# Kernel tuning notes

Measured on AMD Instinct MI355X. Metric: run time of the kernel, lower is better.

The kernel has to match this reference:

```python
import jax, jax.numpy as jnp
import numpy as np

D_MODEL = 1024
NUM_HEADS = 16
HEAD_DIM = D_MODEL // NUM_HEADS
ROPE_BASE = 10000.0


def _rotate_half(x):
    x1, x2 = jnp.split(x, 2, axis=-1)
    return jnp.concatenate([-x2, x1], axis=-1)


def _rope_cache(seq_len, head_dim, dtype):
    half = head_dim // 2
    inv_freq = 1.0 / (ROPE_BASE ** (jnp.arange(half, dtype=jnp.float32) / float(half)))
    t = jnp.arange(seq_len, dtype=jnp.float32)
    freqs = t[:, None] * inv_freq[None, :]          # [s, half]
    emb = jnp.concatenate([freqs, freqs], axis=-1)   # [s, head_dim]
    cos = jnp.cos(emb)[None, None, :, :].astype(dtype)  # [1,1,s,d]
    sin = jnp.sin(emb)[None, None, :, :].astype(dtype)
    return cos, sin


def setup_inputs() -> dict:
    key = jax.random.key(0)
    k1, k2, k3 = jax.random.split(key, 3)
    b, s = 4, 2048
    x = jax.random.normal(k1, (b, s, D_MODEL), dtype=jnp.float32)
    mask = jnp.ones((b, s), dtype=jnp.float32)
    Wqkv = jax.random.normal(k2, (D_MODEL, 3 * D_MODEL), dtype=jnp.float32) * (D_MODEL ** -0.5)
    Wout = jax.random.normal(k3, (D_MODEL, D_MODEL), dtype=jnp.float32) * (D_MODEL ** -0.5)
    return {"x": x, "mask": mask, "Wqkv": Wqkv, "Wout": Wout}


def reference(x, mask, Wqkv, Wout):
    b, s, _ = x.shape
    qkv = x @ Wqkv                                   # [b,s,3*d_model]
    q, k, v = jnp.split(qkv, 3, axis=-1)

    def split_heads(t):
        return t.reshape(b, s, NUM_HEADS, HEAD_DIM).transpose(0, 2, 1, 3)  # [b,h,s,d]

    q, k, v = map(split_heads, (q, k, v))
    cos, sin = _rope_cache(s, HEAD_DIM, x.dtype)
    q = q * cos + _rotate_half(q) * sin
    k = k * cos + _rotate_half(k) * sin

    scale = HEAD_DIM ** -0.5
    logits = jnp.einsum('bhid,bhjd->bhij', q, k) * scale
    logits = logits + (1.0 - mask)[:, None, None, :] * -1e9
    attn = jax.nn.softmax(logits, axis=-1)
    out = jnp.einsum('bhij,bhjd->bhid', attn, v)     # [b,h,s,d]
    out = out.transpose(0, 2, 1, 3).reshape(b, s, D_MODEL)
    return out @ Wout
```

## Files before the change

### kernel.cpp

```cpp
#include <hip/hip_runtime.h>

typedef unsigned short u16;
typedef unsigned int u32;
typedef int i32x2 __attribute__((ext_vector_type(2)));
typedef float f32x4 __attribute__((ext_vector_type(4)));
typedef float f32x16 __attribute__((ext_vector_type(16)));
typedef __bf16 bf16x8 __attribute__((ext_vector_type(8)));
typedef unsigned short u16x8 __attribute__((ext_vector_type(8)));
typedef unsigned short u16x4 __attribute__((ext_vector_type(4)));
typedef unsigned int u32x4 __attribute__((ext_vector_type(4)));

#define S_ 2048
#define DM 1024

#define LDS_U32(p) ((__attribute__((address_space(3))) unsigned int*)(p))
#define GLB_U32(p) ((const __attribute__((address_space(1))) unsigned int*)(p))

__device__ __forceinline__ u16 f2bf(float f) {
    unsigned int u = __float_as_uint(f);
    u += 0x7fffu + ((u >> 16) & 1u);
    return (u16)(u >> 16);
}
__device__ __forceinline__ float bf2f(u16 s) {
    return __uint_as_float(((unsigned int)s) << 16);
}
__device__ __forceinline__ float fast_exp2(float x) {
#if __has_builtin(__builtin_amdgcn_exp2f)
    return __builtin_amdgcn_exp2f(x);
#else
    return __expf(x * 0.69314718056f);
#endif
}

__global__ __launch_bounds__(256) void f32_to_bf16_kernel(const float* __restrict__ in,
                                                          u16* __restrict__ o, int n) {
    int i = (blockIdx.x * 256 + threadIdx.x) << 2;
    if (i >= n) return;
    float4 f = *(const float4*)&in[i];
    u16x4 r;
    r[0] = f2bf(f.x); r[1] = f2bf(f.y); r[2] = f2bf(f.z); r[3] = f2bf(f.w);
    *(u16x4*)&o[i] = r;
}

__global__ __launch_bounds__(256) void transpose_w(const float* __restrict__ W,
                                                   u16* __restrict__ Wt, int K, int N) {
    __shared__ float tile[32][33];
    int nb = blockIdx.x << 5, kb = blockIdx.y << 5;
    int tx = threadIdx.x & 31, ty = threadIdx.x >> 5;
#pragma unroll
    for (int r = 0; r < 32; r += 8)
        tile[ty + r][tx] = W[(size_t)(kb + ty + r) * N + nb + tx];
    __syncthreads();
#pragma unroll
    for (int r = 0; r < 32; r += 8)
        Wt[(size_t)(nb + ty + r) * K + kb + tx] = f2bf(tile[tx][ty + r]);
}


#define ABLK(B, KK) ((B) * 32768 + (KK) * 8192)
#define BBLK(B, KK) ((B) * 32768 + 16384 + (KK) * 8192)

template <int MODE>
__global__ __launch_bounds__(512, 2) void gemm256(const u16* __restrict__ A,
                                                  const u16* __restrict__ Bt,
                                                  float* __restrict__ Cf,
                                                  u16* __restrict__ Qp, u16* __restrict__ Kp,
                                                  u16* __restrict__ Vtp,
                                                  int M, int N, int K) {
    __shared__ __align__(16) u16 lds[65536];
    const int tid = threadIdx.x, wave = tid >> 6, lane = tid & 63;
    const int Ntiles = N >> 8;
    const int cpx = gridDim.x >> 3;
    const int bid = (int)blockIdx.x;
    const int wg = (bid & 7) * cpx + (bid >> 3);
    const int mt = wg / Ntiles, nt = wg % Ntiles;
    const int m0 = mt << 8, n0 = nt << 8;
    const int wm = (wave >> 2) << 7, wn = (wave & 3) << 6;
    const int lr = lane & 15, lu = lane >> 4;

    const int NT = K >> 6;
    const int NIT = K >> 7;

    f32x4 acc[8][4] = {};

    const int srow0 = wave * 16 + (lane >> 2);
    const int scole = (((lane & 3) ^ ((lane >> 3) & 3)) << 3);

#define STAGE(BLK, MAT, ROW0, KCOL)                                                           \
    {                                                                                         \
        _Pragma("unroll") for (int l = 0; l < 2; ++l) {                                       \
            const u16* src = &(MAT)[(size_t)((ROW0) + srow0 + l * 128) * K + (KCOL) + scole];  \
            __builtin_amdgcn_global_load_lds(GLB_U32(src),                                    \
                LDS_U32(&lds[(BLK) + l * 4096 + wave * 512]), 16, 0, 0);                      \
        }                                                                                     \
    }

#define LDFRAG(BLK, ROW) \
    __builtin_bit_cast(bf16x8, *(const u16x8*)&lds[(BLK) + (ROW) * 32 + ((lu ^ (((ROW) >> 1) & 3)) << 3)])

#define PHASE(BUF, IH, KK, LOADB, SBLK, SMAT, SROW0, SKT, SKK, DOVM_END)                  \
    {                                                                                     \
        _Pragma("unroll") for (int ii = 0; ii < 4; ++ii) {                                \
            int row = wm + ((IH) * 4 + ii) * 16 + lr;                                     \
            af[ii] = LDFRAG(ABLK(BUF, KK), row);                                          \
        }                                                                                 \
        if (LOADB) {                                                                      \
            _Pragma("unroll") for (int j = 0; j < 4; ++j) {                               \
                int row = wn + j * 16 + lr;                                               \
                bfv[j] = LDFRAG(BBLK(BUF, KK), row);                                      \
            }                                                                             \
        }                                                                                 \
        STAGE(SBLK, SMAT, SROW0, (((SKT) & (NT - 1)) << 6) + ((SKK) << 5));               \
        asm volatile("s_barrier" ::: "memory");                                           \
        asm volatile("s_waitcnt lgkmcnt(0)" ::: "memory");                                \
        __builtin_amdgcn_sched_barrier(0);                                                \
        __builtin_amdgcn_s_setprio(1);                                                    \
        _Pragma("unroll") for (int ii = 0; ii < 4; ++ii)                                  \
            _Pragma("unroll") for (int j = 0; j < 4; ++j)                                 \
                acc[(IH) * 4 + ii][j] = __builtin_amdgcn_mfma_f32_16x16x32_bf16(          \
                    af[ii], bfv[j], acc[(IH) * 4 + ii][j], 0, 0, 0);                      \
        __builtin_amdgcn_s_setprio(0);                                                    \
        if (DOVM_END) asm volatile("s_waitcnt vmcnt(8)" ::: "memory");                    \
        asm volatile("s_barrier" ::: "memory");                                           \
    }

    STAGE(ABLK(0, 0), A, m0, 0);
    STAGE(BBLK(0, 0), Bt, n0, 0);
    STAGE(ABLK(0, 1), A, m0, 32);
    STAGE(BBLK(0, 1), Bt, n0, 32);
    STAGE(ABLK(1, 0), A, m0, 64);
    STAGE(BBLK(1, 0), Bt, n0, 64);
    asm volatile("s_waitcnt vmcnt(8)" ::: "memory");
    asm volatile("s_barrier" ::: "memory");

    for (int t = 0; t < NIT; ++t) {
        const int kt = 2 * t;
        bf16x8 af[4], bfv[4];
        PHASE(0, 0, 0, true,  ABLK(1, 1), A,  m0, kt + 1, 1, false);
        PHASE(0, 1, 0, false, BBLK(1, 1), Bt, n0, kt + 1, 1, true);
        PHASE(0, 0, 1, true,  ABLK(0, 0), A,  m0, kt + 2, 0, false);
        PHASE(0, 1, 1, false, BBLK(0, 0), Bt, n0, kt + 2, 0, true);
        PHASE(1, 0, 0, true,  ABLK(0, 1), A,  m0, kt + 2, 1, false);
        PHASE(1, 1, 0, false, BBLK(0, 1), Bt, n0, kt + 2, 1, true);
        PHASE(1, 0, 1, true,  ABLK(1, 0), A,  m0, kt + 3, 0, false);
        PHASE(1, 1, 1, false, BBLK(1, 0), Bt, n0, kt + 3, 0, true);
    }

    if (MODE == 0) {
        const int t = (n0 + wn) >> 10;
        if (t < 2) {
            const float LN1E4_32 = 9.210340371976184f / 32.0f;
            const float invf0 = __expf(-(float)lr * LN1E4_32);
            const float invf1 = __expf(-(float)(lr + 16) * LN1E4_32);
#pragma unroll
            for (int i = 0; i < 8; ++i) {
                const int rbase = m0 + wm + (i << 4) + ((lane >> 4) << 2);
#pragma unroll
                for (int jj = 0; jj < 4; ++jj) {
                    const float s = (float)((rbase + jj) & (S_ - 1));
                    float sn0, c0, sn1, c1;
                    __sincosf(s * invf0, &sn0, &c0);
                    __sincosf(s * invf1, &sn1, &c1);
                    const float v0 = acc[i][0][jj], v1 = acc[i][1][jj];
                    const float v2 = acc[i][2][jj], v3 = acc[i][3][jj];
                    acc[i][0][jj] = v0 * c0 - v2 * sn0;
                    acc[i][2][jj] = v2 * c0 + v0 * sn0;
                    acc[i][1][jj] = v1 * c1 - v3 * sn1;
                    acc[i][3][jj] = v3 * c1 + v1 * sn1;
                }
            }
            u16* P = (t == 0) ? Qp : Kp;
#pragma unroll
            for (int i = 0; i < 8; ++i) {
#pragma unroll
                for (int j = 0; j < 4; ++j) {
                    int rbase = m0 + wm + (i << 4) + ((lane >> 4) << 2);
                    int col = n0 + wn + (j << 4) + lr;
                    int h = (col & 1023) >> 6, d = col & 63;
#pragma unroll
                    for (int jj = 0; jj < 4; ++jj) {
                        int row = rbase + jj;
                        int b = row >> 11, s = row & 2047;
                        P[((size_t)((b << 4) + h) * S_ + s) * 64 + d] = f2bf(acc[i][j][jj]);
                    }
                }
            }
        } else {
#pragma unroll
            for (int i = 0; i < 8; ++i) {
                const int rbase = m0 + wm + (i << 4) + ((lane >> 4) << 2);
                const int b = rbase >> 11, sb = rbase & 2047;
#pragma unroll
                for (int j = 0; j < 4; ++j) {
                    int col = n0 + wn + (j << 4) + lr;
                    int h = (col & 1023) >> 6, d = col & 63;
                    u16x4 pk;
#pragma unroll
                    for (int jj = 0; jj < 4; ++jj) pk[jj] = f2bf(acc[i][j][jj]);
                    *(u16x4*)&Vtp[((size_t)((b << 4) + h) * 64 + d) * S_ + sb] = pk;
                }
            }
        }
    } else {
#pragma unroll
        for (int i = 0; i < 8; ++i)
#pragma unroll
            for (int j = 0; j < 4; ++j) {
                int rbase = m0 + wm + (i << 4) + ((lane >> 4) << 2);
                int col = n0 + wn + (j << 4) + lr;
#pragma unroll
                for (int jj = 0; jj < 4; ++jj)
                    Cf[(size_t)(rbase + jj) * N + col] = acc[i][j][jj];
            }
    }
#undef PHASE
#undef LDFRAG
#undef STAGE
}

__device__ __forceinline__ void softmax_chain(f32x16* p, f32x16* acc, f32x16& accS,
                                              float& m_run, u32* wa, u32* wb,
                                              const float* madd_tile, bool hasmask,
                                              float* bcast_w, int c, int hi) {
    if (hasmask) {
#pragma unroll
        for (int tt = 0; tt < 2; ++tt)
#pragma unroll
            for (int rq = 0; rq < 4; ++rq) {
                float4 mf = *(const float4*)&madd_tile[tt * 32 + rq * 8 + hi * 4];
                p[tt][4 * rq + 0] += mf.x;
                p[tt][4 * rq + 1] += mf.y;
                p[tt][4 * rq + 2] += mf.z;
                p[tt][4 * rq + 3] += mf.w;
            }
    }

    float tm[16];
#pragma unroll
    for (int r = 0; r < 16; ++r) tm[r] = fmaxf(p[0][r], p[1][r]);
    float a0 = fmaxf(fmaxf(tm[0], tm[1]), tm[2]);
    float a1 = fmaxf(fmaxf(tm[3], tm[4]), tm[5]);
    float a2 = fmaxf(fmaxf(tm[6], tm[7]), tm[8]);
    float a3 = fmaxf(fmaxf(tm[9], tm[10]), tm[11]);
    float a4 = fmaxf(fmaxf(tm[12], tm[13]), tm[14]);
    float b0 = fmaxf(fmaxf(a0, a1), a2);
    float b1 = fmaxf(fmaxf(a3, a4), tm[15]);
    float mx = fmaxf(b0, b1);
    {
        i32x2 mm = __builtin_amdgcn_permlane32_swap(__float_as_int(mx), __float_as_int(mx), false, false);
        mx = fmaxf(__int_as_float(mm[0]), __int_as_float(mm[1]));
    }

    if (!__all(mx - m_run <= 8.0f)) {
        float mnew = fmaxf(m_run, mx);
        float alpha = fast_exp2(m_run - mnew);
        m_run = mnew;
        bcast_w[c] = alpha;
        float avf[16];
#pragma unroll
        for (int rq = 0; rq < 4; ++rq) {
            float4 t4 = *(const float4*)&bcast_w[rq * 8 + hi * 4];
            avf[4 * rq + 0] = t4.x; avf[4 * rq + 1] = t4.y;
            avf[4 * rq + 2] = t4.z; avf[4 * rq + 3] = t4.w;
        }
#pragma unroll
        for (int r = 0; r < 16; ++r) {
            acc[0][r] *= avf[r];
            acc[1][r] *= avf[r];
            accS[r]   *= avf[r];
        }
    }

#pragma unroll
    for (int tt = 0; tt < 2; ++tt)
#pragma unroll
        for (int r = 0; r < 16; ++r)
            p[tt][r] = fast_exp2(p[tt][r] - m_run);

#pragma unroll
    for (int tt = 0; tt < 2; ++tt)
#pragma unroll
        for (int rq = 0; rq < 4; ++rq) {
            float e0 = p[tt][4 * rq + 0], e1 = p[tt][4 * rq + 1];
            float e2 = p[tt][4 * rq + 2], e3 = p[tt][4 * rq + 3];
            u32 w0, w1;
            asm("v_cvt_pk_bf16_f32 %0, %1, %2" : "=v"(w0) : "v"(e0), "v"(e1));
            asm("v_cvt_pk_bf16_f32 %0, %1, %2" : "=v"(w1) : "v"(e2), "v"(e3));
            wa[4 * tt + rq] = w0;
            wb[4 * tt + rq] = w1;
        }
}

__global__ __launch_bounds__(256, 2) void attn_kernel(const u16* __restrict__ q,
                                                      const u16* __restrict__ k,
                                                      const u16* __restrict__ vt,
                                                      const float* __restrict__ mask,
                                                      u16* __restrict__ outp) {
    __shared__ __align__(16) u16 Kl[2][64 * 64];
    __shared__ __align__(16) u16 Vl[2][64 * 64];
    __shared__ float madd2[2][64];
    __shared__ float bcast[4][32];

    const int tid = threadIdx.x, wave = tid >> 6, lane = tid & 63;
    const int c = lane & 31, hi = lane >> 5, c7 = c & 7;
    const int bh = blockIdx.x & 63, qt = blockIdx.x >> 6;
    const int b = bh >> 4, h = bh & 15;
    const size_t base = (size_t)bh * (S_ * 64);
    const int qrowA = (qt << 8) + (wave << 5) + c;
    const int qrowB = qrowA + 128;

    const float QS = 0.18033688f;

    bf16x8 qfA[4], qfB[4];
#pragma unroll
    for (int j = 0; j < 4; ++j) {
        u16x8 rawA = *(const u16x8*)&q[base + (size_t)qrowA * 64 + j * 16 + hi * 8];
        u16x8 rawB = *(const u16x8*)&q[base + (size_t)qrowB * 64 + j * 16 + hi * 8];
        u16x8 scA, scB;
#pragma unroll
        for (int e = 0; e < 8; ++e) {
            scA[e] = f2bf(bf2f(rawA[e]) * QS);
            scB[e] = f2bf(bf2f(rawB[e]) * QS);
        }
        qfA[j] = __builtin_bit_cast(bf16x8, scA);
        qfB[j] = __builtin_bit_cast(bf16x8, scB);
    }

    u16x8 ou;
#pragma unroll
    for (int e = 0; e < 8; ++e) ou[e] = 0x3F80;
    const bf16x8 onesf = __builtin_bit_cast(bf16x8, ou);

    f32x16 accA[2] = {}, accB[2] = {};
    f32x16 accSA = {}, accSB = {};
    float m_runA = -1e30f, m_runB = -1e30f;

    const int sr = tid >> 2, su = (tid & 3) << 1;
    const int so0 = sr * 64 + ((su ^ (sr & 7)) << 3);
    const int so1 = sr * 64 + (((su + 1) ^ (sr & 7)) << 3);

    u16x8 kc0 = *(const u16x8*)&k[base + (size_t)sr * 64 + su * 8];
    u16x8 kc1 = *(const u16x8*)&k[base + (size_t)sr * 64 + su * 8 + 8];
    u16x8 vc0 = *(const u16x8*)&vt[base + (size_t)sr * S_ + su * 8];
    u16x8 vc1 = *(const u16x8*)&vt[base + (size_t)sr * S_ + su * 8 + 8];
    float mval = (tid < 64) ? mask[b * S_ + tid] : 1.0f;

    for (int t = 0; t < 32; ++t) {
        const int bi = t & 1;
        u16* Kb = &Kl[bi][0];
        u16* Vb = &Vl[bi][0];
        *(u16x8*)&Kb[so0] = kc0;
        *(u16x8*)&Kb[so1] = kc1;
        *(u16x8*)&Vb[so0] = vc0;
        *(u16x8*)&Vb[so1] = vc1;
        if (tid < 64) madd2[bi][tid] = (1.0f - mval) * -1.44269504e9f;
        if (t + 1 < 32) {
            const int kn = (t + 1) << 6;
            kc0 = *(const u16x8*)&k[base + (size_t)(kn + sr) * 64 + su * 8];
            kc1 = *(const u16x8*)&k[base + (size_t)(kn + sr) * 64 + su * 8 + 8];
            vc0 = *(const u16x8*)&vt[base + (size_t)sr * S_ + kn + su * 8];
            vc1 = *(const u16x8*)&vt[base + (size_t)sr * S_ + kn + su * 8 + 8];
            mval = (tid < 64) ? mask[b * S_ + kn + tid] : 1.0f;
        }
        __syncthreads();

        f32x16 pA[2] = {}, pB[2] = {};
        __builtin_amdgcn_s_setprio(1);
#pragma unroll
        for (int j = 0; j < 4; ++j) {
            const int uo = ((2 * j + hi) ^ c7) << 3;
            bf16x8 ka  = __builtin_bit_cast(bf16x8, *(const u16x8*)&Kb[c * 64 + uo]);
            bf16x8 kb2 = __builtin_bit_cast(bf16x8, *(const u16x8*)&Kb[(32 + c) * 64 + uo]);
            pA[0] = __builtin_amdgcn_mfma_f32_32x32x16_bf16(ka,  qfA[j], pA[0], 0, 0, 0);
            pA[1] = __builtin_amdgcn_mfma_f32_32x32x16_bf16(kb2, qfA[j], pA[1], 0, 0, 0);
            pB[0] = __builtin_amdgcn_mfma_f32_32x32x16_bf16(ka,  qfB[j], pB[0], 0, 0, 0);
            pB[1] = __builtin_amdgcn_mfma_f32_32x32x16_bf16(kb2, qfB[j], pB[1], 0, 0, 0);
        }
        __builtin_amdgcn_s_setprio(0);

        bool hasmask = __any(madd2[bi][lane] != 0.0f);

        u32 waA[8], wbA[8], waB[8], wbB[8];
        softmax_chain(pA, accA, accSA, m_runA, waA, wbA, &madd2[bi][0], hasmask, &bcast[wave][0], c, hi);
        softmax_chain(pB, accB, accSB, m_runB, waB, wbB, &madd2[bi][0], hasmask, &bcast[wave][0], c, hi);

        __builtin_amdgcn_s_setprio(1);
#pragma unroll
        for (int ks = 0; ks < 4; ++ks) {
            i32x2 raA = __builtin_amdgcn_permlane32_swap((int)waA[2 * ks], (int)waA[2 * ks + 1], false, false);
            i32x2 rbA = __builtin_amdgcn_permlane32_swap((int)wbA[2 * ks], (int)wbA[2 * ks + 1], false, false);
            i32x2 raB = __builtin_amdgcn_permlane32_swap((int)waB[2 * ks], (int)waB[2 * ks + 1], false, false);
            i32x2 rbB = __builtin_amdgcn_permlane32_swap((int)wbB[2 * ks], (int)wbB[2 * ks + 1], false, false);
            u32x4 pwA, pwB;
            pwA[0] = (u32)raA[0]; pwA[1] = (u32)rbA[0]; pwA[2] = (u32)raA[1]; pwA[3] = (u32)rbA[1];
            pwB[0] = (u32)raB[0]; pwB[1] = (u32)rbB[0]; pwB[2] = (u32)raB[1]; pwB[3] = (u32)rbB[1];
            bf16x8 pafA = __builtin_bit_cast(bf16x8, pwA);
            bf16x8 pafB = __builtin_bit_cast(bf16x8, pwB);
            accSA = __builtin_amdgcn_mfma_f32_32x32x16_bf16(pafA, onesf, accSA, 0, 0, 0);
            accSB = __builtin_amdgcn_mfma_f32_32x32x16_bf16(pafB, onesf, accSB, 0, 0, 0);
            const int uo = ((2 * ks + hi) ^ c7) << 3;
#pragma unroll
            for (int dt = 0; dt < 2; ++dt) {
                bf16x8 vf = __builtin_bit_cast(bf16x8,
                            *(const u16x8*)&Vb[(32 * dt + c) * 64 + uo]);
                accA[dt] = __builtin_amdgcn_mfma_f32_32x32x16_bf16(pafA, vf, accA[dt], 0, 0, 0);
                accB[dt] = __builtin_amdgcn_mfma_f32_32x32x16_bf16(pafB, vf, accB[dt], 0, 0, 0);
            }
        }
        __builtin_amdgcn_s_setprio(0);
    }

    {
        const size_t orow0 = (size_t)b * S_ + (qt << 8) + (wave << 5);
#pragma unroll
        for (int dt = 0; dt < 2; ++dt)
#pragma unroll
            for (int r = 0; r < 16; ++r) {
                int qr = (r & 3) + 8 * (r >> 2) + 4 * hi;
                outp[(orow0 + qr) * DM + h * 64 + dt * 32 + c] =
                    f2bf(accA[dt][r] * __builtin_amdgcn_rcpf(accSA[r]));
            }
    }
    {
        const size_t orow0 = (size_t)b * S_ + (qt << 8) + (wave << 5) + 128;
#pragma unroll
        for (int dt = 0; dt < 2; ++dt)
#pragma unroll
            for (int r = 0; r < 16; ++r) {
                int qr = (r & 3) + 8 * (r >> 2) + 4 * hi;
                outp[(orow0 + qr) * DM + h * 64 + dt * 32 + c] =
                    f2bf(accB[dt][r] * __builtin_amdgcn_rcpf(accSB[r]));
            }
    }
}

extern "C" void kernel_launch(void* const* d_in, const int* in_sizes, int n_in,
                              void* d_out, int out_size, void* d_ws, size_t ws_size,
                              hipStream_t stream) {
    const float* x    = (const float*)d_in[0];
    const float* mask = (const float*)d_in[1];
    const float* Wqkv = (const float*)d_in[2];
    const float* Wout = (const float*)d_in[3];
    float* out = (float*)d_out;
    char* ws = (char*)d_ws;
    const size_t MB = 1u << 20;
    u16* xb    = (u16*)(ws);
    u16* WqkvT = (u16*)(ws + 16 * MB);
    u16* WoutT = (u16*)(ws + 22 * MB);
    u16* qb    = (u16*)(ws + 24 * MB);
    u16* kb    = (u16*)(ws + 40 * MB);
    u16* vtb   = (u16*)(ws + 56 * MB);
    u16* ao    = xb;

    f32_to_bf16_kernel<<<8192, 256, 0, stream>>>(x, xb, 8192 * 1024);
    transpose_w<<<dim3(96, 32), 256, 0, stream>>>(Wqkv, WqkvT, 1024, 3072);
    transpose_w<<<dim3(32, 32), 256, 0, stream>>>(Wout, WoutT, 1024, 1024);
    gemm256<0><<<32 * 12, 512, 0, stream>>>(xb, WqkvT, nullptr, qb, kb, vtb, 8192, 3072, 1024);
    attn_kernel<<<512, 256, 0, stream>>>(qb, kb, vtb, mask, ao);
    gemm256<1><<<32 * 4, 512, 0, stream>>>(ao, WoutT, out, nullptr, nullptr, nullptr, 8192, 1024, 1024);
}
```

Before: 210.7 us.

## Shrink GEMM tile to 128x256 to double workgroup count

Changes the GEMM block tile from 256x256 to 128x256. The grid doubles for both the QKV and output projections, and each wave now holds a 4x4 accumulator set. The per-K-step pipeline drops from eight half phases to four full phases with one A load and two B loads each, and the vmcnt waits are adjusted to match. LDS use per block falls. The aim is better load balance across CUs, since the old 128-block output GEMM left much of the device idle, at the cost of lower arithmetic intensity per block.

```diff
diff --git a/kernel.cpp b/kernel.cpp
--- a/kernel.cpp
+++ b/kernel.cpp
@@ -57,8 +57,8 @@
 }
 
 
-#define ABLK(B, KK) ((B) * 32768 + (KK) * 8192)
-#define BBLK(B, KK) ((B) * 32768 + 16384 + (KK) * 8192)
+#define ABLK(B, KK) ((B) * 24576 + (KK) * 4096)
+#define BBLK(B, KK) ((B) * 24576 + 8192 + (KK) * 8192)
 
 template <int MODE>
 __global__ __launch_bounds__(512, 2) void gemm256(const u16* __restrict__ A,
@@ -67,83 +67,83 @@
                                                   u16* __restrict__ Qp, u16* __restrict__ Kp,
                                                   u16* __restrict__ Vtp,
                                                   int M, int N, int K) {
-    __shared__ __align__(16) u16 lds[65536];
+    __shared__ __align__(16) u16 lds[49152];
     const int tid = threadIdx.x, wave = tid >> 6, lane = tid & 63;
     const int Ntiles = N >> 8;
     const int cpx = gridDim.x >> 3;
     const int bid = (int)blockIdx.x;
     const int wg = (bid & 7) * cpx + (bid >> 3);
     const int mt = wg / Ntiles, nt = wg % Ntiles;
-    const int m0 = mt << 8, n0 = nt << 8;
-    const int wm = (wave >> 2) << 7, wn = (wave & 3) << 6;
+    const int m0 = mt << 7, n0 = nt << 8;
+    const int wm = (wave >> 2) << 6, wn = (wave & 3) << 6;
     const int lr = lane & 15, lu = lane >> 4;
 
     const int NT = K >> 6;
     const int NIT = K >> 7;
 
-    f32x4 acc[8][4] = {};
+    f32x4 acc[4][4] = {};
 
     const int srow0 = wave * 16 + (lane >> 2);
     const int scole = (((lane & 3) ^ ((lane >> 3) & 3)) << 3);
 
-#define STAGE(BLK, MAT, ROW0, KCOL)                                                           \
-    {                                                                                         \
-        _Pragma("unroll") for (int l = 0; l < 2; ++l) {                                       \
-            const u16* src = &(MAT)[(size_t)((ROW0) + srow0 + l * 128) * K + (KCOL) + scole];  \
-            __builtin_amdgcn_global_load_lds(GLB_U32(src),                                    \
-                LDS_U32(&lds[(BLK) + l * 4096 + wave * 512]), 16, 0, 0);                      \
-        }                                                                                     \
+#define STAGE_A(BLK, KCOL)                                                                \
+    {                                                                                     \
+        const u16* src = &A[(size_t)(m0 + srow0) * K + (KCOL) + scole];                   \
+        __builtin_amdgcn_global_load_lds(GLB_U32(src),                                    \
+            LDS_U32(&lds[(BLK) + wave * 512]), 16, 0, 0);                                 \
+    }
+#define STAGE_B(BLK, KCOL)                                                                \
+    {                                                                                     \
+        _Pragma("unroll") for (int l = 0; l < 2; ++l) {                                   \
+            const u16* src = &Bt[(size_t)(n0 + srow0 + l * 128) * K + (KCOL) + scole];    \
+            __builtin_amdgcn_global_load_lds(GLB_U32(src),                                \
+                LDS_U32(&lds[(BLK) + l * 4096 + wave * 512]), 16, 0, 0);                  \
+        }                                                                                 \
     }
 
 #define LDFRAG(BLK, ROW) \
     __builtin_bit_cast(bf16x8, *(const u16x8*)&lds[(BLK) + (ROW) * 32 + ((lu ^ (((ROW) >> 1) & 3)) << 3)])
 
-#define PHASE(BUF, IH, KK, LOADB, SBLK, SMAT, SROW0, SKT, SKK, DOVM_END)                  \
+#define PHASE(BUF, KK, SBUF, SKK, SKT)                                                    \
     {                                                                                     \
-        _Pragma("unroll") for (int ii = 0; ii < 4; ++ii) {                                \
-            int row = wm + ((IH) * 4 + ii) * 16 + lr;                                     \
-            af[ii] = LDFRAG(ABLK(BUF, KK), row);                                          \
+        _Pragma("unroll") for (int ii = 0; ii < 4; ++ii)                                  \
+            af[ii] = LDFRAG(ABLK(BUF, KK), wm + ii * 16 + lr);                            \
+        _Pragma("unroll") for (int j = 0; j < 4; ++j)                                     \
+            bfv[j] = LDFRAG(BBLK(BUF, KK), wn + j * 16 + lr);                             \
+        {                                                                                 \
+            const int kcol = (((SKT) & (NT - 1)) << 6) + ((SKK) << 5);                    \
+            STAGE_A(ABLK(SBUF, SKK), kcol);                                               \
+            STAGE_B(BBLK(SBUF, SKK), kcol);                                               \
         }                                                                                 \
-        if (LOADB) {                                                                      \
-            _Pragma("unroll") for (int j = 0; j < 4; ++j) {                               \
-                int row = wn + j * 16 + lr;                                               \
-                bfv[j] = LDFRAG(BBLK(BUF, KK), row);                                      \
-            }                                                                             \
-        }                                                                                 \
-        STAGE(SBLK, SMAT, SROW0, (((SKT) & (NT - 1)) << 6) + ((SKK) << 5));               \
         asm volatile("s_barrier" ::: "memory");                                           \
         asm volatile("s_waitcnt lgkmcnt(0)" ::: "memory");                                \
         __builtin_amdgcn_sched_barrier(0);                                                \
         __builtin_amdgcn_s_setprio(1);                                                    \
         _Pragma("unroll") for (int ii = 0; ii < 4; ++ii)                                  \
             _Pragma("unroll") for (int j = 0; j < 4; ++j)                                 \
-                acc[(IH) * 4 + ii][j] = __builtin_amdgcn_mfma_f32_16x16x32_bf16(          \
-                    af[ii], bfv[j], acc[(IH) * 4 + ii][j], 0, 0, 0);                      \
+                acc[ii][j] = __builtin_amdgcn_mfma_f32_16x16x32_bf16(                     \
+                    af[ii], bfv[j], acc[ii][j], 0, 0, 0);                                 \
         __builtin_amdgcn_s_setprio(0);                                                    \
-        if (DOVM_END) asm volatile("s_waitcnt vmcnt(8)" ::: "memory");                    \
+        asm volatile("s_waitcnt vmcnt(6)" ::: "memory");                                  \
         asm volatile("s_barrier" ::: "memory");                                           \
     }
 
-    STAGE(ABLK(0, 0), A, m0, 0);
-    STAGE(BBLK(0, 0), Bt, n0, 0);
-    STAGE(ABLK(0, 1), A, m0, 32);
-    STAGE(BBLK(0, 1), Bt, n0, 32);
-    STAGE(ABLK(1, 0), A, m0, 64);
-    STAGE(BBLK(1, 0), Bt, n0, 64);
-    asm volatile("s_waitcnt vmcnt(8)" ::: "memory");
+    STAGE_A(ABLK(0, 0), 0);
+    STAGE_B(BBLK(0, 0), 0);
+    STAGE_A(ABLK(0, 1), 32);
+    STAGE_B(BBLK(0, 1), 32);
+    STAGE_A(ABLK(1, 0), 64);
+    STAGE_B(BBLK(1, 0), 64);
+    asm volatile("s_waitcnt vmcnt(6)" ::: "memory");
     asm volatile("s_barrier" ::: "memory");
 
     for (int t = 0; t < NIT; ++t) {
         const int kt = 2 * t;
         bf16x8 af[4], bfv[4];
-        PHASE(0, 0, 0, true,  ABLK(1, 1), A,  m0, kt + 1, 1, false);
-        PHASE(0, 1, 0, false, BBLK(1, 1), Bt, n0, kt + 1, 1, true);
-        PHASE(0, 0, 1, true,  ABLK(0, 0), A,  m0, kt + 2, 0, false);
-        PHASE(0, 1, 1, false, BBLK(0, 0), Bt, n0, kt + 2, 0, true);
-        PHASE(1, 0, 0, true,  ABLK(0, 1), A,  m0, kt + 2, 1, false);
-        PHASE(1, 1, 0, false, BBLK(0, 1), Bt, n0, kt + 2, 1, true);
-        PHASE(1, 0, 1, true,  ABLK(1, 0), A,  m0, kt + 3, 0, false);
-        PHASE(1, 1, 1, false, BBLK(1, 0), Bt, n0, kt + 3, 0, true);
+        PHASE(0, 0, 1, 1, kt + 1);
+        PHASE(0, 1, 0, 0, kt + 2);
+        PHASE(1, 0, 0, 1, kt + 2);
+        PHASE(1, 1, 1, 0, kt + 3);
     }
 
     if (MODE == 0) {
@@ -153,7 +153,7 @@
             const float invf0 = __expf(-(float)lr * LN1E4_32);
             const float invf1 = __expf(-(float)(lr + 16) * LN1E4_32);
 #pragma unroll
-            for (int i = 0; i < 8; ++i) {
+            for (int i = 0; i < 4; ++i) {
                 const int rbase = m0 + wm + (i << 4) + ((lane >> 4) << 2);
 #pragma unroll
                 for (int jj = 0; jj < 4; ++jj) {
@@ -171,7 +171,7 @@
             }
             u16* P = (t == 0) ? Qp : Kp;
 #pragma unroll
-            for (int i = 0; i < 8; ++i) {
+            for (int i = 0; i < 4; ++i) {
 #pragma unroll
                 for (int j = 0; j < 4; ++j) {
                     int rbase = m0 + wm + (i << 4) + ((lane >> 4) << 2);
@@ -187,7 +187,7 @@
             }
         } else {
 #pragma unroll
-            for (int i = 0; i < 8; ++i) {
+            for (int i = 0; i < 4; ++i) {
                 const int rbase = m0 + wm + (i << 4) + ((lane >> 4) << 2);
                 const int b = rbase >> 11, sb = rbase & 2047;
 #pragma unroll
@@ -203,7 +203,7 @@
         }
     } else {
 #pragma unroll
-        for (int i = 0; i < 8; ++i)
+        for (int i = 0; i < 4; ++i)
 #pragma unroll
             for (int j = 0; j < 4; ++j) {
                 int rbase = m0 + wm + (i << 4) + ((lane >> 4) << 2);
@@ -215,7 +215,8 @@
     }
 #undef PHASE
 #undef LDFRAG
-#undef STAGE
+#undef STAGE_B
+#undef STAGE_A
 }
 
 __device__ __forceinline__ void softmax_chain(f32x16* p, f32x16* acc, f32x16& accS,
@@ -455,7 +456,7 @@
     f32_to_bf16_kernel<<<8192, 256, 0, stream>>>(x, xb, 8192 * 1024);
     transpose_w<<<dim3(96, 32), 256, 0, stream>>>(Wqkv, WqkvT, 1024, 3072);
     transpose_w<<<dim3(32, 32), 256, 0, stream>>>(Wout, WoutT, 1024, 1024);
-    gemm256<0><<<32 * 12, 512, 0, stream>>>(xb, WqkvT, nullptr, qb, kb, vtb, 8192, 3072, 1024);
+    gemm256<0><<<64 * 12, 512, 0, stream>>>(xb, WqkvT, nullptr, qb, kb, vtb, 8192, 3072, 1024);
     attn_kernel<<<512, 256, 0, stream>>>(qb, kb, vtb, mask, ao);
-    gemm256<1><<<32 * 4, 512, 0, stream>>>(ao, WoutT, out, nullptr, nullptr, nullptr, 8192, 1024, 1024);
-}
+    gemm256<1><<<64 * 4, 512, 0, stream>>>(ao, WoutT, out, nullptr, nullptr, nullptr, 8192, 1024, 1024);
+}
```

New measurement: 204.9 us. 1.03x faster.
